# Kernel tuning notes

Measured on AMD Instinct MI355X. Metric: run time of the kernel, lower is better.

The kernel has to match this reference:

```python
import jax, jax.numpy as jnp
import numpy as np
from jax import lax

B, S, H = 64, 128, 64
EPS = 1e-5


def _conv1d(x, w, b):
    # x: [B, Cin, S], w: [Cout, Cin, 3], padding=1
    y = lax.conv_general_dilated(x, w, window_strides=(1,), padding=[(1, 1)],
                                 dimension_numbers=("NCH", "OIH", "NCH"))
    return y + b[None, :, None]


def _bn(x, g, b, m, v):
    # eval-mode BatchNorm1d over channel dim of [B, C, S]
    inv = g / jnp.sqrt(v + EPS)
    return x * inv[None, :, None] + (b - m * inv)[None, :, None]


def setup_inputs() -> dict:
    key = jax.random.key(0)
    ks = jax.random.split(key, 24)
    d = {}
    d["x"] = jax.random.normal(ks[0], (B, S, 1), dtype=jnp.float32)
    sc = 0.1
    d["conv1_w"] = jax.random.normal(ks[1], (H, 1, 3), dtype=jnp.float32) * sc
    d["conv1_b"] = jax.random.normal(ks[2], (H,), dtype=jnp.float32) * sc
    d["bn1_g"] = jax.random.uniform(ks[3], (H,), dtype=jnp.float32) + 0.5
    d["bn1_b"] = jax.random.normal(ks[4], (H,), dtype=jnp.float32) * sc
    d["bn1_m"] = jax.random.normal(ks[5], (H,), dtype=jnp.float32) * sc
    d["bn1_v"] = jax.random.uniform(ks[6], (H,), dtype=jnp.float32) + 0.5
    d["conv2_w"] = jax.random.normal(ks[7], (H, H, 3), dtype=jnp.float32) * 0.05
    d["conv2_b"] = jax.random.normal(ks[8], (H,), dtype=jnp.float32) * sc
    d["bn2_g"] = jax.random.uniform(ks[9], (H,), dtype=jnp.float32) + 0.5
    d["bn2_b"] = jax.random.normal(ks[10], (H,), dtype=jnp.float32) * sc
    d["bn2_m"] = jax.random.normal(ks[11], (H,), dtype=jnp.float32) * sc
    d["bn2_v"] = jax.random.uniform(ks[12], (H,), dtype=jnp.float32) + 0.5
    d["gat_W"] = jax.random.normal(ks[13], (H, H), dtype=jnp.float32) * 0.05
    d["gat_Wb"] = jax.random.normal(ks[14], (H,), dtype=jnp.float32) * sc
    d["gat_a1"] = jax.random.normal(ks[15], (H,), dtype=jnp.float32) * sc
    d["gat_a2"] = jax.random.normal(ks[16], (H,), dtype=jnp.float32) * sc
    d["gat_ab"] = jax.random.normal(ks[17], (), dtype=jnp.float32) * sc
    d["ta_W"] = jax.random.normal(ks[18], (H, H), dtype=jnp.float32) * 0.05
    d["ta_b"] = jax.random.normal(ks[19], (H,), dtype=jnp.float32) * sc
    d["p1_W"] = jax.random.normal(ks[20], (32, H), dtype=jnp.float32) * sc
    d["p1_b"] = jax.random.normal(ks[21], (32,), dtype=jnp.float32) * sc
    d["p2_W"] = jax.random.normal(ks[22], (1, 32), dtype=jnp.float32) * sc
    d["p2_b"] = jax.random.normal(ks[23], (1,), dtype=jnp.float32) * sc
    return d


def reference(x, conv1_w, conv1_b, bn1_g, bn1_b, bn1_m, bn1_v,
              conv2_w, conv2_b, bn2_g, bn2_b, bn2_m, bn2_v,
              gat_W, gat_Wb, gat_a1, gat_a2, gat_ab,
              ta_W, ta_b, p1_W, p1_b, p2_W, p2_b):
    b, s, _ = x.shape
    # feature extraction: [B, 1, S] -> [B, H, S]
    h = jnp.transpose(x, (0, 2, 1))
    h = jax.nn.relu(_bn(_conv1d(h, conv1_w, conv1_b), bn1_g, bn1_b, bn1_m, bn1_v))
    h = jax.nn.relu(_bn(_conv1d(h, conv2_w, conv2_b), bn2_g, bn2_b, bn2_m, bn2_v))
    # flatten to N = B*S nodes of dim H
    xf = jnp.transpose(h, (0, 2, 1)).reshape(b * s, H)  # [N, H]
    # dense adjacency: softmax(xf xf^T) over rows (single chunk since B<=100)
    adj = jax.nn.softmax(xf @ xf.T, axis=1)  # [N, N]
    # GAT layer; pairwise score decomposed: a([Wh_i;Wh_j]) = Wh_i.a1 + Wh_j.a2 + b
    Wh = xf @ gat_W.T + gat_Wb  # [N, H]
    s1 = Wh @ gat_a1  # [N]
    s2 = Wh @ gat_a2  # [N]
    e = jax.nn.leaky_relu(s1[:, None] + s2[None, :] + gat_ab, 0.2)  # [N, N]
    e = jnp.where(adj > 0, e, jnp.float32(-9e15))
    att = jax.nn.softmax(e, axis=1)
    hp = att @ Wh  # [N, H]
    h2 = hp.reshape(b, s, H)
    # time attention over feature dim
    tw = jax.nn.softmax(h2 @ ta_W.T + ta_b, axis=2)
    h2 = h2 * tw
    # global average pool over sequence
    pooled = jnp.mean(h2, axis=1)  # [B, H]
    out = jax.nn.relu(pooled @ p1_W.T + p1_b) @ p2_W.T + p2_b  # [B, 1]
    return out
```

## Files before the change

kernel.cpp:

```cpp
#include <hip/hip_runtime.h>
#include <hip/hip_bf16.h>

#define Hd 64
#define Sd 128
#define Bd 64
#define Nn 8192
#define EPSd 1e-5f

__device__ __forceinline__ float wred_sum(float v) {
    for (int m = 32; m; m >>= 1) v += __shfl_xor(v, m);
    return v;
}
__device__ __forceinline__ float wred_max(float v) {
    for (int m = 32; m; m >>= 1) v = fmaxf(v, __shfl_xor(v, m));
    return v;
}
__device__ __forceinline__ float wscan_incl(float x, int lane) {
    #pragma unroll
    for (int d = 1; d < 64; d <<= 1) {
        float t = __shfl_up(x, d);
        if (lane >= d) x += t;
    }
    return x;
}

__global__ __launch_bounds__(256) void k1_features(
        const float* __restrict__ x,
        const float* __restrict__ c1w, const float* __restrict__ c1b,
        const float* __restrict__ b1g, const float* __restrict__ b1b,
        const float* __restrict__ b1m, const float* __restrict__ b1v,
        const float* __restrict__ c2w, const float* __restrict__ c2b,
        const float* __restrict__ b2g, const float* __restrict__ b2b,
        const float* __restrict__ b2m, const float* __restrict__ b2v,
        float* __restrict__ xf) {
    __shared__ float h1[34 * 64];
    __shared__ float wtk[3 * 16 * 64 * 4];
    int b  = blockIdx.x >> 2;
    int s0 = (blockIdx.x & 3) * 32;
    int tid = threadIdx.x;
    for (int idx = tid; idx < 12288; idx += 256) {
        int j    = idx & 3;
        int c    = (idx >> 2) & 63;
        int cin4 = (idx >> 8) & 15;
        int k    = idx >> 12;
        wtk[idx] = c2w[(c * 64 + cin4 * 4 + j) * 3 + k];
    }
    for (int idx = tid; idx < 34 * 64; idx += 256) {
        int cin = idx & 63;
        int col = idx >> 6;
        int s   = s0 - 1 + col;
        float v = 0.f;
        if (s >= 0 && s < Sd) {
            float xm = (s > 0)      ? x[b * Sd + s - 1] : 0.f;
            float x0 = x[b * Sd + s];
            float xp = (s < Sd - 1) ? x[b * Sd + s + 1] : 0.f;
            float y  = c1w[cin * 3 + 0] * xm + c1w[cin * 3 + 1] * x0 + c1w[cin * 3 + 2] * xp + c1b[cin];
            float inv = b1g[cin] * rsqrtf(b1v[cin] + EPSd);
            v = fmaxf(y * inv + (b1b[cin] - b1m[cin] * inv), 0.f);
        }
        h1[col * 64 + cin] = v;
    }
    __syncthreads();
    int c = tid & 63, g = tid >> 6;
    float inv2 = b2g[c] * rsqrtf(b2v[c] + EPSd);
    float sh2  = b2b[c] - b2m[c] * inv2;
    float acc[8];
    #pragma unroll
    for (int p = 0; p < 8; ++p) acc[p] = c2b[c];
    const float4* h14 = (const float4*)h1;
    const float4* wt4 = (const float4*)wtk;
    for (int cin4 = 0; cin4 < 16; ++cin4) {
        float4 xs[10];
        #pragma unroll
        for (int q = 0; q < 10; ++q) xs[q] = h14[(g * 8 + q) * 16 + cin4];
        #pragma unroll
        for (int k = 0; k < 3; ++k) {
            float4 w4 = wt4[(k * 16 + cin4) * 64 + c];
            #pragma unroll
            for (int p = 0; p < 8; ++p) {
                float4 x4 = xs[p + k];
                acc[p] += w4.x * x4.x + w4.y * x4.y + w4.z * x4.z + w4.w * x4.w;
            }
        }
    }
    #pragma unroll
    for (int p = 0; p < 8; ++p) {
        int sl = g * 8 + p;
        float outv = fmaxf(acc[p] * inv2 + sh2, 0.f);
        xf[(b * Sd + s0 + sl) * 64 + c] = outv;
    }
}

__global__ __launch_bounds__(256) void k2_wh(
        const float* __restrict__ xf,
        const float* __restrict__ gW, const float* __restrict__ gWb,
        const float* __restrict__ a1, const float* __restrict__ a2,
        float* __restrict__ Wh, float* __restrict__ s1, float* __restrict__ s2) {
    __shared__ float4 WT4[1024];
    __shared__ float4 xr4[256];
    int tid = threadIdx.x;
    int node0 = blockIdx.x * 16;
    for (int fidx = tid; fidx < 1024; fidx += 256) {
        int h_ = fidx >> 4, kk4 = fidx & 15;
        WT4[kk4 * 64 + h_] = ((const float4*)gW)[fidx];
    }
    xr4[tid] = ((const float4*)(xf + node0 * 64))[tid];
    __syncthreads();
    int h = tid & 63, w = tid >> 6;
    float bias = gWb[h];
    float acc0 = bias, acc1 = bias, acc2 = bias, acc3 = bias;
    #pragma unroll
    for (int kk4 = 0; kk4 < 16; ++kk4) {
        float4 w4 = WT4[kk4 * 64 + h];
        float4 xa = xr4[(w * 4 + 0) * 16 + kk4];
        float4 xb = xr4[(w * 4 + 1) * 16 + kk4];
        float4 xc = xr4[(w * 4 + 2) * 16 + kk4];
        float4 xd = xr4[(w * 4 + 3) * 16 + kk4];
        acc0 += w4.x * xa.x + w4.y * xa.y + w4.z * xa.z + w4.w * xa.w;
        acc1 += w4.x * xb.x + w4.y * xb.y + w4.z * xb.z + w4.w * xb.w;
        acc2 += w4.x * xc.x + w4.y * xc.y + w4.z * xc.z + w4.w * xc.w;
        acc3 += w4.x * xd.x + w4.y * xd.y + w4.z * xd.z + w4.w * xd.w;
    }
    float va1 = a1[h], va2 = a2[h];
    float accs[4] = {acc0, acc1, acc2, acc3};
    #pragma unroll
    for (int r = 0; r < 4; ++r) {
        int n = node0 + w * 4 + r;
        Wh[n * 64 + h] = accs[r];
        float r1 = wred_sum(accs[r] * va1);
        float r2 = wred_sum(accs[r] * va2);
        if (h == 0) { s1[n] = r1; s2[n] = r2; }
    }
}

__global__ __launch_bounds__(256) void k4_rank(const float* __restrict__ s2,
                                               int* __restrict__ rankPart,
                                               float* __restrict__ pmax) {
    __shared__ float4 ts4[64];
    int bid = blockIdx.x;
    int jg = bid >> 5, part = bid & 31;
    int tid = threadIdx.x;
    if (tid < 64) ts4[tid] = ((const float4*)(s2 + part * 256))[tid];
    __syncthreads();
    if (jg == 0 && tid < 64) {
        float4 t4 = ts4[tid];
        float m = fmaxf(fmaxf(t4.x, t4.y), fmaxf(t4.z, t4.w));
        m = wred_max(m);
        if (tid == 0) pmax[part] = m;
    }
    int j = jg * 256 + tid;
    float tj = s2[j];
    int jloc = j - part * 256;
    int cnt = 0;
    #pragma unroll 4
    for (int q = 0; q < 64; ++q) {
        float4 t4 = ts4[q];
        int rb = q * 4;
        cnt += (t4.x < tj || (t4.x == tj && rb     < jloc)) ? 1 : 0;
        cnt += (t4.y < tj || (t4.y == tj && rb + 1 < jloc)) ? 1 : 0;
        cnt += (t4.z < tj || (t4.z == tj && rb + 2 < jloc)) ? 1 : 0;
        cnt += (t4.w < tj || (t4.w == tj && rb + 3 < jloc)) ? 1 : 0;
    }
    rankPart[part * 8192 + j] = cnt;
}

__global__ __launch_bounds__(256) void k5_scatter(
        const float* __restrict__ Wh, const float* __restrict__ s2,
        const int* __restrict__ rankPart,
        float* __restrict__ Rpos, float* __restrict__ Rneg,
        float* __restrict__ spos, float* __restrict__ sneg,
        float* __restrict__ tsorted) {
    int fidx = blockIdx.x * 256 + threadIdx.x;
    int j = fidx >> 4, h4 = fidx & 15;
    int r = 0;
    #pragma unroll
    for (int p = 0; p < 32; ++p) r += rankPart[p * 8192 + j];
    float t = s2[j];
    float e1 = expf(t), e2 = expf(0.2f * t);
    float4 wv = ((const float4*)Wh)[fidx];
    ((float4*)Rpos)[r * 16 + h4] = make_float4(e1 * wv.x, e1 * wv.y, e1 * wv.z, e1 * wv.w);
    ((float4*)Rneg)[r * 16 + h4] = make_float4(e2 * wv.x, e2 * wv.y, e2 * wv.z, e2 * wv.w);
    if (h4 == 0) { spos[r] = e1; sneg[r] = e2; tsorted[r] = t; }
}

__global__ __launch_bounds__(256) void k6_csum(
        const float* __restrict__ Rpos, const float* __restrict__ Rneg,
        const float* __restrict__ spos, const float* __restrict__ sneg,
        float* __restrict__ csP, float* __restrict__ csN,
        float* __restrict__ csp, float* __restrict__ csn) {
    __shared__ float ldsP[4][64], ldsN[4][64];
    int ch = blockIdx.x, tid = threadIdx.x;
    int h = tid & 63, w = tid >> 6;
    int rb = ch * 128 + w * 32;
    double aP = 0.0, aN = 0.0;
    #pragma unroll
    for (int r = 0; r < 32; ++r) {
        aP += Rpos[(rb + r) * 64 + h];
        aN += Rneg[(rb + r) * 64 + h];
    }
    ldsP[w][h] = (float)aP; ldsN[w][h] = (float)aN;
    __syncthreads();
    if (w == 0) {
        csP[ch * 64 + h] = ldsP[0][h] + ldsP[1][h] + ldsP[2][h] + ldsP[3][h];
    } else if (w == 1) {
        csN[ch * 64 + h] = ldsN[0][h] + ldsN[1][h] + ldsN[2][h] + ldsN[3][h];
    } else if (w == 2) {
        float v = spos[ch * 128 + h] + spos[ch * 128 + 64 + h];
        v = wred_sum(v);
        if (h == 0) csp[ch] = v;
    } else {
        float v = sneg[ch * 128 + h] + sneg[ch * 128 + 64 + h];
        v = wred_sum(v);
        if (h == 0) csn[ch] = v;
    }
}

__global__ __launch_bounds__(256) void k8_expand(
        const float* __restrict__ Rpos, const float* __restrict__ Rneg,
        const float* __restrict__ spos, const float* __restrict__ sneg,
        const float* __restrict__ csP, const float* __restrict__ csN,
        const float* __restrict__ csp, const float* __restrict__ csn,
        float* __restrict__ Ppos, float* __restrict__ Pneg,
        float* __restrict__ ppos, float* __restrict__ pneg) {
    __shared__ float ldsA[4][64], ldsB[4][64];
    __shared__ float cbPs[64], cbNs[64];
    int ch = blockIdx.x, tid = threadIdx.x;
    int h = tid & 63, w = tid >> 6;
    double bp = 0.0, bn = 0.0;
    for (int p = w; p < ch; p += 4) { bp += csP[p * 64 + h]; bn += csN[p * 64 + h]; }
    ldsA[w][h] = (float)bp; ldsB[w][h] = (float)bn;
    __syncthreads();
    if (w == 0) {
        cbPs[h] = ldsA[0][h] + ldsA[1][h] + ldsA[2][h] + ldsA[3][h];
        cbNs[h] = ldsB[0][h] + ldsB[1][h] + ldsB[2][h] + ldsB[3][h];
    }
    __syncthreads();
    float cbP = cbPs[h], cbN = cbNs[h];
    int rb = ch * 128 + w * 32;
    float v[32];
    #pragma unroll
    for (int r = 0; r < 32; ++r) v[r] = Rpos[(rb + r) * 64 + h];
    double acc = 0.0;
    #pragma unroll
    for (int r = 0; r < 32; ++r) acc += v[r];
    ldsA[w][h] = (float)acc;
    __syncthreads();
    float off = cbP;
    #pragma unroll
    for (int w2 = 0; w2 < 4; ++w2) if (w2 < w) off += ldsA[w2][h];
    double a2_ = 0.0;
    #pragma unroll
    for (int r = 0; r < 32; ++r) { Ppos[(rb + r) * 64 + h] = off + (float)a2_; a2_ += v[r]; }
    if (ch == 63 && w == 3) Ppos[Nn * 64 + h] = off + (float)a2_;
    __syncthreads();
    #pragma unroll
    for (int r = 0; r < 32; ++r) v[r] = Rneg[(rb + r) * 64 + h];
    acc = 0.0;
    #pragma unroll
    for (int r = 0; r < 32; ++r) acc += v[r];
    ldsB[w][h] = (float)acc;
    __syncthreads();
    off = cbN;
    #pragma unroll
    for (int w2 = 0; w2 < 4; ++w2) if (w2 < w) off += ldsB[w2][h];
    a2_ = 0.0;
    #pragma unroll
    for (int r = 0; r < 32; ++r) { Pneg[(rb + r) * 64 + h] = off + (float)a2_; a2_ += v[r]; }
    if (ch == 63 && w == 3) Pneg[Nn * 64 + h] = off + (float)a2_;
    if (w == 0) {
        int lane = h;
        float bs = (lane < ch) ? csp[lane] : 0.f;
        bs = wred_sum(bs);
        float v0 = spos[ch * 128 + lane], v1 = spos[ch * 128 + 64 + lane];
        float i0 = wscan_incl(v0, lane);
        float t0 = __shfl(i0, 63);
        float i1 = wscan_incl(v1, lane);
        ppos[ch * 128 + lane]      = bs + i0 - v0;
        ppos[ch * 128 + 64 + lane] = bs + t0 + i1 - v1;
        if (ch == 63 && lane == 63) ppos[Nn] = bs + t0 + i1;
    } else if (w == 1) {
        int lane = h;
        float bs = (lane < ch) ? csn[lane] : 0.f;
        bs = wred_sum(bs);
        float v0 = sneg[ch * 128 + lane], v1 = sneg[ch * 128 + 64 + lane];
        float i0 = wscan_incl(v0, lane);
        float t0 = __shfl(i0, 63);
        float i1 = wscan_incl(v1, lane);
        pneg[ch * 128 + lane]      = bs + i0 - v0;
        pneg[ch * 128 + 64 + lane] = bs + t0 + i1 - v1;
        if (ch == 63 && lane == 63) pneg[Nn] = bs + t0 + i1;
    }
}

__global__ __launch_bounds__(256) void k9a_node(
        const float* __restrict__ s1, const float* __restrict__ tsorted,
        const float* __restrict__ pmax, const float* __restrict__ gab,
        const float* __restrict__ Ppos, const float* __restrict__ Pneg,
        const float* __restrict__ ppos, const float* __restrict__ pneg,
        const float* __restrict__ taW, const float* __restrict__ tab,
        float* __restrict__ h2) {
    __shared__ float4 wt4[1024];
    __shared__ float tso[8192];
    __shared__ float hl[16 * 64];
    int tid = threadIdx.x;
    for (int fidx = tid; fidx < 1024; fidx += 256) {
        int h_ = fidx >> 4, kk4 = fidx & 15;
        wt4[kk4 * 64 + h_] = ((const float4*)taW)[fidx];
    }
    for (int i = tid; i < 2048; i += 256)
        ((float4*)tso)[i] = ((const float4*)tsorted)[i];
    float tmx = pmax[tid & 31];
    tmx = wred_max(tmx);
    __syncthreads();
    int h = tid & 63, w = tid >> 6;
    float gabv = gab[0];
    float tabv = tab[h];
    float Tp  = Ppos[Nn * 64 + h];
    float ppT = ppos[Nn];
    for (int r = 0; r < 4; ++r) {
        int n = blockIdx.x * 16 + w * 4 + r;
        float c = s1[n] + gabv;
        float negc = -c;
        int k = 0;
        #pragma unroll
        for (int stp = 4096; stp > 0; stp >>= 1)
            if (tso[k + stp - 1] <= negc) k += stp;
        if (k == 8191 && tso[8191] <= negc) k = 8192;
        float z = c + tmx;
        float m = (z >= 0.f) ? z : 0.2f * z;
        float E1 = expf(c - m), E2 = expf(0.2f * c - m);
        float Pp = Ppos[k * 64 + h], Pn = Pneg[k * 64 + h];
        float num = E1 * (Tp - Pp) + E2 * Pn;
        float den = E1 * (ppT - ppos[k]) + E2 * pneg[k];
        float hp = num / den;
        int slot = w * 4 + r;
        hl[slot * 64 + h] = hp;
        float vv = tabv;
        const float4* hlr = (const float4*)&hl[slot * 64];
        #pragma unroll
        for (int kk4 = 0; kk4 < 16; ++kk4) {
            float4 w4 = wt4[kk4 * 64 + h];
            float4 x4 = hlr[kk4];
            vv += w4.x * x4.x + w4.y * x4.y + w4.z * x4.z + w4.w * x4.w;
        }
        float mx = wred_max(vv);
        float e = expf(vv - mx);
        float se = wred_sum(e);
        h2[n * 64 + h] = hp * (e / se);
    }
}

__global__ __launch_bounds__(256) void k9b_pool(
        const float* __restrict__ h2,
        const float* __restrict__ p1W, const float* __restrict__ p1b,
        const float* __restrict__ p2W, const float* __restrict__ p2b,
        float* __restrict__ out) {
    __shared__ float pacc[4 * 64];
    __shared__ float pl[64];
    __shared__ float p1s[32 * 65];
    int tid = threadIdx.x, b = blockIdx.x;
    int w = tid >> 6, h = tid & 63;
    for (int idx = tid; idx < 2048; idx += 256) {
        int q = idx >> 6, kk = idx & 63;
        p1s[q * 65 + kk] = p1W[idx];
    }
    float a = 0.f;
    for (int s = w * 32; s < w * 32 + 32; ++s) a += h2[(b * Sd + s) * 64 + h];
    pacc[w * 64 + h] = a;
    __syncthreads();
    if (w == 0) {
        float pooled = (pacc[h] + pacc[64 + h] + pacc[128 + h] + pacc[192 + h]) * (1.f / 128.f);
        pl[h] = pooled;
        float val = 0.f;
        if (h < 32) {
            float acc = p1b[h];
            #pragma unroll
            for (int kk = 0; kk < 64; ++kk) acc += p1s[h * 65 + kk] * pl[kk];
            val = p2W[h] * fmaxf(acc, 0.f);
        }
        val = wred_sum(val);
        if (h == 0) out[b] = val + p2b[0];
    }
}

extern "C" void kernel_launch(void* const* d_in, const int* in_sizes, int n_in,
                              void* d_out, int out_size, void* d_ws, size_t ws_size,
                              hipStream_t stream) {
    const float* x    = (const float*)d_in[0];
    const float* c1w  = (const float*)d_in[1];
    const float* c1b  = (const float*)d_in[2];
    const float* b1g  = (const float*)d_in[3];
    const float* b1b  = (const float*)d_in[4];
    const float* b1m  = (const float*)d_in[5];
    const float* b1v  = (const float*)d_in[6];
    const float* c2w  = (const float*)d_in[7];
    const float* c2b  = (const float*)d_in[8];
    const float* b2g  = (const float*)d_in[9];
    const float* b2b  = (const float*)d_in[10];
    const float* b2m  = (const float*)d_in[11];
    const float* b2v  = (const float*)d_in[12];
    const float* gW   = (const float*)d_in[13];
    const float* gWb  = (const float*)d_in[14];
    const float* ga1  = (const float*)d_in[15];
    const float* ga2  = (const float*)d_in[16];
    const float* gab  = (const float*)d_in[17];
    const float* taW  = (const float*)d_in[18];
    const float* tab  = (const float*)d_in[19];
    const float* p1W  = (const float*)d_in[20];
    const float* p1b  = (const float*)d_in[21];
    const float* p2W  = (const float*)d_in[22];
    const float* p2b  = (const float*)d_in[23];
    float* out = (float*)d_out;

    float* ws = (float*)d_ws;
    float* xf      = ws;
    float* Wh      = xf + 524288;
    float* s1      = Wh + 524288;
    float* s2v     = s1 + 8192;
    float* tsorted = s2v + 8192;
    float* spos    = tsorted + 8192;
    float* sneg    = spos + 8192;
    float* ppos    = sneg + 8192;
    float* pneg    = ppos + 8256;
    float* csP     = pneg + 8256;
    float* csN     = csP + 4096;
    float* csp     = csN + 4096;
    float* csn     = csp + 64;
    float* pmax    = csn + 64;
    int*   rankPart= (int*)(pmax + 64);
    float* Rpos    = (float*)(rankPart + 262144);
    float* Rneg    = Rpos + 524288;
    float* Ppos    = Rneg + 524288;
    float* Pneg    = Ppos + 524352;
    float* h2      = Rpos;

    k1_features<<<256, 256, 0, stream>>>(x, c1w, c1b, b1g, b1b, b1m, b1v,
                                         c2w, c2b, b2g, b2b, b2m, b2v, xf);
    k2_wh<<<512, 256, 0, stream>>>(xf, gW, gWb, ga1, ga2, Wh, s1, s2v);
    k4_rank<<<1024, 256, 0, stream>>>(s2v, rankPart, pmax);
    k5_scatter<<<512, 256, 0, stream>>>(Wh, s2v, rankPart, Rpos, Rneg, spos, sneg, tsorted);
    k6_csum<<<64, 256, 0, stream>>>(Rpos, Rneg, spos, sneg, csP, csN, csp, csn);
    k8_expand<<<64, 256, 0, stream>>>(Rpos, Rneg, spos, sneg, csP, csN, csp, csn,
                                      Ppos, Pneg, ppos, pneg);
    k9a_node<<<512, 256, 0, stream>>>(s1, tsorted, pmax, gab, Ppos, Pneg, ppos, pneg,
                                      taW, tab, h2);
    k9b_pool<<<64, 256, 0, stream>>>(h2, p1W, p1b, p2W, p2b, out);
}
```

Before: 69.52 us.

## Fuse feature extraction with Wh projection and compute thresholds in rank kernel

Merges the conv/BN feature kernel with the GAT linear projection so the intermediate node features stay in shared memory instead of making a round trip through global memory. The per-node binary search over sorted s2 in the node kernel is replaced by a threshold count computed alongside the rank counts in the rank kernel and reduced in the scatter kernel. The scatter kernel now sums partial ranks through shared memory. This removes one launch and the node kernel's large shared-memory copy of the sorted array, at the cost of an extra 1MB partial-count buffer and more work in the rank kernel.

```diff
diff --git a/kernel.cpp b/kernel.cpp
--- a/kernel.cpp
+++ b/kernel.cpp
@@ -24,7 +24,7 @@
     return x;
 }
 
-__global__ __launch_bounds__(256) void k1_features(
+__global__ __launch_bounds__(256) void kA_feat_wh(
         const float* __restrict__ x,
         const float* __restrict__ c1w, const float* __restrict__ c1b,
         const float* __restrict__ b1g, const float* __restrict__ b1b,
@@ -32,9 +32,12 @@
         const float* __restrict__ c2w, const float* __restrict__ c2b,
         const float* __restrict__ b2g, const float* __restrict__ b2b,
         const float* __restrict__ b2m, const float* __restrict__ b2v,
-        float* __restrict__ xf) {
-    __shared__ float h1[34 * 64];
-    __shared__ float wtk[3 * 16 * 64 * 4];
+        const float* __restrict__ gW, const float* __restrict__ gWb,
+        const float* __restrict__ a1, const float* __restrict__ a2,
+        float* __restrict__ Wh, float* __restrict__ s1, float* __restrict__ s2) {
+    __shared__ float buf[14464];
+    float* h1  = buf;
+    float* wtk = buf + 2176;
     int b  = blockIdx.x >> 2;
     int s0 = (blockIdx.x & 3) * 32;
     int tid = threadIdx.x;
@@ -67,75 +70,63 @@
     float acc[8];
     #pragma unroll
     for (int p = 0; p < 8; ++p) acc[p] = c2b[c];
-    const float4* h14 = (const float4*)h1;
-    const float4* wt4 = (const float4*)wtk;
-    for (int cin4 = 0; cin4 < 16; ++cin4) {
-        float4 xs[10];
-        #pragma unroll
-        for (int q = 0; q < 10; ++q) xs[q] = h14[(g * 8 + q) * 16 + cin4];
-        #pragma unroll
-        for (int k = 0; k < 3; ++k) {
-            float4 w4 = wt4[(k * 16 + cin4) * 64 + c];
+    {
+        const float4* h14 = (const float4*)h1;
+        const float4* wt4 = (const float4*)wtk;
+        for (int cin4 = 0; cin4 < 16; ++cin4) {
+            float4 xs[10];
             #pragma unroll
-            for (int p = 0; p < 8; ++p) {
-                float4 x4 = xs[p + k];
-                acc[p] += w4.x * x4.x + w4.y * x4.y + w4.z * x4.z + w4.w * x4.w;
+            for (int q = 0; q < 10; ++q) xs[q] = h14[(g * 8 + q) * 16 + cin4];
+            #pragma unroll
+            for (int k = 0; k < 3; ++k) {
+                float4 w4 = wt4[(k * 16 + cin4) * 64 + c];
+                #pragma unroll
+                for (int p = 0; p < 8; ++p) {
+                    float4 x4 = xs[p + k];
+                    acc[p] += w4.x * x4.x + w4.y * x4.y + w4.z * x4.z + w4.w * x4.w;
+                }
             }
         }
     }
-    #pragma unroll
-    for (int p = 0; p < 8; ++p) {
-        int sl = g * 8 + p;
-        float outv = fmaxf(acc[p] * inv2 + sh2, 0.f);
-        xf[(b * Sd + s0 + sl) * 64 + c] = outv;
-    }
-}
-
-__global__ __launch_bounds__(256) void k2_wh(
-        const float* __restrict__ xf,
-        const float* __restrict__ gW, const float* __restrict__ gWb,
-        const float* __restrict__ a1, const float* __restrict__ a2,
-        float* __restrict__ Wh, float* __restrict__ s1, float* __restrict__ s2) {
-    __shared__ float4 WT4[1024];
-    __shared__ float4 xr4[256];
-    int tid = threadIdx.x;
-    int node0 = blockIdx.x * 16;
+    __syncthreads();
+    float*  xfl  = buf;
+    float4* gWT4 = (float4*)(buf + 2176);
+    #pragma unroll
+    for (int p = 0; p < 8; ++p)
+        xfl[(g * 8 + p) * 64 + c] = fmaxf(acc[p] * inv2 + sh2, 0.f);
     for (int fidx = tid; fidx < 1024; fidx += 256) {
         int h_ = fidx >> 4, kk4 = fidx & 15;
-        WT4[kk4 * 64 + h_] = ((const float4*)gW)[fidx];
-    }
-    xr4[tid] = ((const float4*)(xf + node0 * 64))[tid];
+        gWT4[kk4 * 64 + h_] = ((const float4*)gW)[fidx];
+    }
     __syncthreads();
     int h = tid & 63, w = tid >> 6;
-    float bias = gWb[h];
-    float acc0 = bias, acc1 = bias, acc2 = bias, acc3 = bias;
-    #pragma unroll
-    for (int kk4 = 0; kk4 < 16; ++kk4) {
-        float4 w4 = WT4[kk4 * 64 + h];
-        float4 xa = xr4[(w * 4 + 0) * 16 + kk4];
-        float4 xb = xr4[(w * 4 + 1) * 16 + kk4];
-        float4 xc = xr4[(w * 4 + 2) * 16 + kk4];
-        float4 xd = xr4[(w * 4 + 3) * 16 + kk4];
-        acc0 += w4.x * xa.x + w4.y * xa.y + w4.z * xa.z + w4.w * xa.w;
-        acc1 += w4.x * xb.x + w4.y * xb.y + w4.z * xb.z + w4.w * xb.w;
-        acc2 += w4.x * xc.x + w4.y * xc.y + w4.z * xc.z + w4.w * xc.w;
-        acc3 += w4.x * xd.x + w4.y * xd.y + w4.z * xd.z + w4.w * xd.w;
-    }
-    float va1 = a1[h], va2 = a2[h];
-    float accs[4] = {acc0, acc1, acc2, acc3};
-    #pragma unroll
-    for (int r = 0; r < 4; ++r) {
-        int n = node0 + w * 4 + r;
-        Wh[n * 64 + h] = accs[r];
-        float r1 = wred_sum(accs[r] * va1);
-        float r2 = wred_sum(accs[r] * va2);
+    float4 wreg[16];
+    #pragma unroll
+    for (int kk4 = 0; kk4 < 16; ++kk4) wreg[kk4] = gWT4[kk4 * 64 + h];
+    float va1 = a1[h], va2 = a2[h], bias = gWb[h];
+    const float4* xf4 = (const float4*)xfl;
+    int n0 = b * Sd + s0;
+    for (int q = 0; q < 8; ++q) {
+        int sl = w * 8 + q;
+        float accw = bias;
+        #pragma unroll
+        for (int kk4 = 0; kk4 < 16; ++kk4) {
+            float4 x4 = xf4[sl * 16 + kk4];
+            accw += wreg[kk4].x * x4.x + wreg[kk4].y * x4.y + wreg[kk4].z * x4.z + wreg[kk4].w * x4.w;
+        }
+        int n = n0 + sl;
+        Wh[n * 64 + h] = accw;
+        float r1 = wred_sum(accw * va1);
+        float r2 = wred_sum(accw * va2);
         if (h == 0) { s1[n] = r1; s2[n] = r2; }
     }
 }
 
-__global__ __launch_bounds__(256) void k4_rank(const float* __restrict__ s2,
-                                               int* __restrict__ rankPart,
-                                               float* __restrict__ pmax) {
+__global__ __launch_bounds__(256) void kB_rank(
+        const float* __restrict__ s2, const float* __restrict__ s1,
+        const float* __restrict__ gab,
+        int* __restrict__ rankPart, int* __restrict__ kPart,
+        float* __restrict__ pmax) {
     __shared__ float4 ts4[64];
     int bid = blockIdx.x;
     int jg = bid >> 5, part = bid & 31;
@@ -150,40 +141,61 @@
     }
     int j = jg * 256 + tid;
     float tj = s2[j];
+    float negc = -(s1[j] + gab[0]);
     int jloc = j - part * 256;
-    int cnt = 0;
+    int cntR = 0, cntK = 0;
     #pragma unroll 4
     for (int q = 0; q < 64; ++q) {
         float4 t4 = ts4[q];
         int rb = q * 4;
-        cnt += (t4.x < tj || (t4.x == tj && rb     < jloc)) ? 1 : 0;
-        cnt += (t4.y < tj || (t4.y == tj && rb + 1 < jloc)) ? 1 : 0;
-        cnt += (t4.z < tj || (t4.z == tj && rb + 2 < jloc)) ? 1 : 0;
-        cnt += (t4.w < tj || (t4.w == tj && rb + 3 < jloc)) ? 1 : 0;
-    }
-    rankPart[part * 8192 + j] = cnt;
-}
-
-__global__ __launch_bounds__(256) void k5_scatter(
+        cntR += (t4.x < tj || (t4.x == tj && rb     < jloc)) ? 1 : 0;
+        cntR += (t4.y < tj || (t4.y == tj && rb + 1 < jloc)) ? 1 : 0;
+        cntR += (t4.z < tj || (t4.z == tj && rb + 2 < jloc)) ? 1 : 0;
+        cntR += (t4.w < tj || (t4.w == tj && rb + 3 < jloc)) ? 1 : 0;
+        cntK += (t4.x <= negc) ? 1 : 0;
+        cntK += (t4.y <= negc) ? 1 : 0;
+        cntK += (t4.z <= negc) ? 1 : 0;
+        cntK += (t4.w <= negc) ? 1 : 0;
+    }
+    rankPart[part * 8192 + j] = cntR;
+    kPart[part * 8192 + j]    = cntK;
+}
+
+__global__ __launch_bounds__(256) void kC_scatter(
         const float* __restrict__ Wh, const float* __restrict__ s2,
-        const int* __restrict__ rankPart,
+        const int* __restrict__ rankPart, const int* __restrict__ kPart,
         float* __restrict__ Rpos, float* __restrict__ Rneg,
         float* __restrict__ spos, float* __restrict__ sneg,
-        float* __restrict__ tsorted) {
-    int fidx = blockIdx.x * 256 + threadIdx.x;
-    int j = fidx >> 4, h4 = fidx & 15;
-    int r = 0;
-    #pragma unroll
-    for (int p = 0; p < 32; ++p) r += rankPart[p * 8192 + j];
+        int* __restrict__ kk) {
+    __shared__ int rsl[512], ksl[512];
+    __shared__ int rsum[16], ksum[16];
+    int tid = threadIdx.x;
+    int j0 = blockIdx.x * 16;
+    for (int idx = tid; idx < 512; idx += 256) {
+        int p = idx >> 4, jj = idx & 15;
+        rsl[idx] = rankPart[p * 8192 + j0 + jj];
+        ksl[idx] = kPart[p * 8192 + j0 + jj];
+    }
+    __syncthreads();
+    if (tid < 16) {
+        int a = 0, bq = 0;
+        #pragma unroll
+        for (int p = 0; p < 32; ++p) { a += rsl[p * 16 + tid]; bq += ksl[p * 16 + tid]; }
+        rsum[tid] = a; ksum[tid] = bq;
+    }
+    __syncthreads();
+    int jj = tid >> 4, h4 = tid & 15;
+    int j = j0 + jj;
+    int r = rsum[jj];
     float t = s2[j];
     float e1 = expf(t), e2 = expf(0.2f * t);
-    float4 wv = ((const float4*)Wh)[fidx];
+    float4 wv = ((const float4*)Wh)[j * 16 + h4];
     ((float4*)Rpos)[r * 16 + h4] = make_float4(e1 * wv.x, e1 * wv.y, e1 * wv.z, e1 * wv.w);
     ((float4*)Rneg)[r * 16 + h4] = make_float4(e2 * wv.x, e2 * wv.y, e2 * wv.z, e2 * wv.w);
-    if (h4 == 0) { spos[r] = e1; sneg[r] = e2; tsorted[r] = t; }
-}
-
-__global__ __launch_bounds__(256) void k6_csum(
+    if (h4 == 0) { spos[r] = e1; sneg[r] = e2; kk[j] = ksum[jj]; }
+}
+
+__global__ __launch_bounds__(256) void kD_csum(
         const float* __restrict__ Rpos, const float* __restrict__ Rneg,
         const float* __restrict__ spos, const float* __restrict__ sneg,
         float* __restrict__ csP, float* __restrict__ csN,
@@ -215,7 +227,7 @@
     }
 }
 
-__global__ __launch_bounds__(256) void k8_expand(
+__global__ __launch_bounds__(256) void kE_expand(
         const float* __restrict__ Rpos, const float* __restrict__ Rneg,
         const float* __restrict__ spos, const float* __restrict__ sneg,
         const float* __restrict__ csP, const float* __restrict__ csN,
@@ -292,23 +304,20 @@
     }
 }
 
-__global__ __launch_bounds__(256) void k9a_node(
-        const float* __restrict__ s1, const float* __restrict__ tsorted,
+__global__ __launch_bounds__(256) void kF_node(
+        const float* __restrict__ s1, const int* __restrict__ kk,
         const float* __restrict__ pmax, const float* __restrict__ gab,
         const float* __restrict__ Ppos, const float* __restrict__ Pneg,
         const float* __restrict__ ppos, const float* __restrict__ pneg,
         const float* __restrict__ taW, const float* __restrict__ tab,
         float* __restrict__ h2) {
     __shared__ float4 wt4[1024];
-    __shared__ float tso[8192];
     __shared__ float hl[16 * 64];
     int tid = threadIdx.x;
     for (int fidx = tid; fidx < 1024; fidx += 256) {
         int h_ = fidx >> 4, kk4 = fidx & 15;
         wt4[kk4 * 64 + h_] = ((const float4*)taW)[fidx];
     }
-    for (int i = tid; i < 2048; i += 256)
-        ((float4*)tso)[i] = ((const float4*)tsorted)[i];
     float tmx = pmax[tid & 31];
     tmx = wred_max(tmx);
     __syncthreads();
@@ -320,12 +329,7 @@
     for (int r = 0; r < 4; ++r) {
         int n = blockIdx.x * 16 + w * 4 + r;
         float c = s1[n] + gabv;
-        float negc = -c;
-        int k = 0;
-        #pragma unroll
-        for (int stp = 4096; stp > 0; stp >>= 1)
-            if (tso[k + stp - 1] <= negc) k += stp;
-        if (k == 8191 && tso[8191] <= negc) k = 8192;
+        int k = kk[n];
         float z = c + tmx;
         float m = (z >= 0.f) ? z : 0.2f * z;
         float E1 = expf(c - m), E2 = expf(0.2f * c - m);
@@ -350,7 +354,7 @@
     }
 }
 
-__global__ __launch_bounds__(256) void k9b_pool(
+__global__ __launch_bounds__(256) void kG_pool(
         const float* __restrict__ h2,
         const float* __restrict__ p1W, const float* __restrict__ p1b,
         const float* __restrict__ p2W, const float* __restrict__ p2b,
@@ -361,8 +365,8 @@
     int tid = threadIdx.x, b = blockIdx.x;
     int w = tid >> 6, h = tid & 63;
     for (int idx = tid; idx < 2048; idx += 256) {
-        int q = idx >> 6, kk = idx & 63;
-        p1s[q * 65 + kk] = p1W[idx];
+        int q = idx >> 6, kq = idx & 63;
+        p1s[q * 65 + kq] = p1W[idx];
     }
     float a = 0.f;
     for (int s = w * 32; s < w * 32 + 32; ++s) a += h2[(b * Sd + s) * 64 + h];
@@ -375,7 +379,7 @@
         if (h < 32) {
             float acc = p1b[h];
             #pragma unroll
-            for (int kk = 0; kk < 64; ++kk) acc += p1s[h * 65 + kk] * pl[kk];
+            for (int kq = 0; kq < 64; ++kq) acc += p1s[h * 65 + kq] * pl[kq];
             val = p2W[h] * fmaxf(acc, 0.f);
         }
         val = wred_sum(val);
@@ -413,12 +417,10 @@
     float* out = (float*)d_out;
 
     float* ws = (float*)d_ws;
-    float* xf      = ws;
-    float* Wh      = xf + 524288;
+    float* Wh      = ws;
     float* s1      = Wh + 524288;
     float* s2v     = s1 + 8192;
-    float* tsorted = s2v + 8192;
-    float* spos    = tsorted + 8192;
+    float* spos    = s2v + 8192;
     float* sneg    = spos + 8192;
     float* ppos    = sneg + 8192;
     float* pneg    = ppos + 8256;
@@ -427,22 +429,25 @@
     float* csp     = csN + 4096;
     float* csn     = csp + 64;
     float* pmax    = csn + 64;
-    int*   rankPart= (int*)(pmax + 64);
-    float* Rpos    = (float*)(rankPart + 262144);
+    int*   kk      = (int*)(pmax + 64);
+    int*   rankPart= kk + 8192;
+    int*   kPart   = rankPart + 262144;
+    float* Rpos    = (float*)(kPart + 262144);
     float* Rneg    = Rpos + 524288;
     float* Ppos    = Rneg + 524288;
     float* Pneg    = Ppos + 524352;
     float* h2      = Rpos;
 
-    k1_features<<<256, 256, 0, stream>>>(x, c1w, c1b, b1g, b1b, b1m, b1v,
-                                         c2w, c2b, b2g, b2b, b2m, b2v, xf);
-    k2_wh<<<512, 256, 0, stream>>>(xf, gW, gWb, ga1, ga2, Wh, s1, s2v);
-    k4_rank<<<1024, 256, 0, stream>>>(s2v, rankPart, pmax);
-    k5_scatter<<<512, 256, 0, stream>>>(Wh, s2v, rankPart, Rpos, Rneg, spos, sneg, tsorted);
-    k6_csum<<<64, 256, 0, stream>>>(Rpos, Rneg, spos, sneg, csP, csN, csp, csn);
-    k8_expand<<<64, 256, 0, stream>>>(Rpos, Rneg, spos, sneg, csP, csN, csp, csn,
+    kA_feat_wh<<<256, 256, 0, stream>>>(x, c1w, c1b, b1g, b1b, b1m, b1v,
+                                        c2w, c2b, b2g, b2b, b2m, b2v,
+                                        gW, gWb, ga1, ga2, Wh, s1, s2v);
+    kB_rank<<<1024, 256, 0, stream>>>(s2v, s1, gab, rankPart, kPart, pmax);
+    kC_scatter<<<512, 256, 0, stream>>>(Wh, s2v, rankPart, kPart,
+                                        Rpos, Rneg, spos, sneg, kk);
+    kD_csum<<<64, 256, 0, stream>>>(Rpos, Rneg, spos, sneg, csP, csN, csp, csn);
+    kE_expand<<<64, 256, 0, stream>>>(Rpos, Rneg, spos, sneg, csP, csN, csp, csn,
                                       Ppos, Pneg, ppos, pneg);
-    k9a_node<<<512, 256, 0, stream>>>(s1, tsorted, pmax, gab, Ppos, Pneg, ppos, pneg,
-                                      taW, tab, h2);
-    k9b_pool<<<64, 256, 0, stream>>>(h2, p1W, p1b, p2W, p2b, out);
-}
+    kF_node<<<512, 256, 0, stream>>>(s1, kk, pmax, gab, Ppos, Pneg, ppos, pneg,
+                                     taW, tab, h2);
+    kG_pool<<<64, 256, 0, stream>>>(h2, p1W, p1b, p2W, p2b, out);
+}
```

Measured after the change: 68.57 us. Within noise of the previous version (-1.4%).
